# Performance work log

Measured on AMD Instinct MI355X. Metric: run time of the kernel, lower is better.

Reference implementation:

```python
import jax, jax.numpy as jnp
import numpy as np

N_NODES = 100000
N_EDGES = 400000
N_GRAPHS = 2048
F_IN = 78
HEADS1 = 10
OUT2 = 128


def _gat_conv(x, src, dst, W, a_src, a_dst, b, heads, out_dim):
    """PyG-style GATConv with self-loops already included in (src, dst)."""
    N = x.shape[0]
    h = (x @ W).reshape(N, heads, out_dim)                       # [N,H,D]
    alpha_src = jnp.einsum('nhd,hd->nh', h, a_src)               # [N,H]
    alpha_dst = jnp.einsum('nhd,hd->nh', h, a_dst)               # [N,H]
    e = jax.nn.leaky_relu(alpha_src[src] + alpha_dst[dst], 0.2)  # [E,H]
    # ragged softmax over incoming edges per destination node
    m = jax.ops.segment_max(e, dst, num_segments=N)
    m = jnp.where(jnp.isfinite(m), m, 0.0)
    ex = jnp.exp(e - jax.lax.stop_gradient(m)[dst])
    denom = jax.ops.segment_sum(ex, dst, num_segments=N)
    alpha = ex / (denom[dst] + 1e-16)                            # [E,H]
    msg = h[src] * alpha[:, :, None]                             # [E,H,D]
    out = jax.ops.segment_sum(msg, dst, num_segments=N)          # [N,H,D]
    return out.reshape(N, heads * out_dim) + b


def setup_inputs() -> dict:
    key = jax.random.key(0)
    ks = jax.random.split(key, 24)
    p = lambda k, shape: (jax.random.normal(k, shape, dtype=jnp.float32) * 0.05)
    x = jax.random.normal(ks[0], (N_NODES, F_IN), dtype=jnp.float32)
    edge_index = jax.random.randint(ks[1], (2, N_EDGES), 0, N_NODES, dtype=jnp.int32)
    # sorted batch assignment guaranteeing every graph is non-empty
    batch = ((jnp.arange(N_NODES, dtype=jnp.int32) * N_GRAPHS) // N_NODES).astype(jnp.int32)
    target = jax.random.normal(ks[2], (N_GRAPHS, 1280), dtype=jnp.float32)
    return {
        'x': x, 'edge_index': edge_index, 'batch': batch, 'target': target,
        'W1': p(ks[3], (F_IN, HEADS1 * F_IN)),
        'a_src1': p(ks[4], (HEADS1, F_IN)),
        'a_dst1': p(ks[5], (HEADS1, F_IN)),
        'b1': jnp.zeros((HEADS1 * F_IN,), jnp.float32),
        'W2': p(ks[6], (HEADS1 * F_IN, OUT2)),
        'a_src2': p(ks[7], (1, OUT2)),
        'a_dst2': p(ks[8], (1, OUT2)),
        'b2': jnp.zeros((OUT2,), jnp.float32),
        'w_gate': p(ks[9], (OUT2, 1)),
        'b_gate': jnp.zeros((1,), jnp.float32),
        'W_xt': p(ks[10], (1280, 256)),
        'b_xt': jnp.zeros((256,), jnp.float32),
        'W_fc1': p(ks[11], (512, 1024)),
        'b_fc1': jnp.zeros((1024,), jnp.float32),
        'W_fc2': p(ks[12], (1024, 256)),
        'b_fc2': jnp.zeros((256,), jnp.float32),
        'W_out': p(ks[13], (256, 1)),
        'b_out': jnp.zeros((1,), jnp.float32),
    }


def reference(x, edge_index, batch, target, W1, a_src1, a_dst1, b1,
              W2, a_src2, a_dst2, b2, w_gate, b_gate, W_xt, b_xt,
              W_fc1, b_fc1, W_fc2, b_fc2, W_out, b_out):
    N = x.shape[0]
    loop = jnp.arange(N, dtype=edge_index.dtype)
    src = jnp.concatenate([edge_index[0], loop])   # add self-loops (PyG default)
    dst = jnp.concatenate([edge_index[1], loop])

    h = jax.nn.elu(_gat_conv(x, src, dst, W1, a_src1, a_dst1, b1, HEADS1, F_IN))
    h = _gat_conv(h, src, dst, W2, a_src2, a_dst2, b2, 1, OUT2)
    h = jax.nn.relu(h)                              # [N,128]

    # WeightedSumAndMax readout
    w = jax.nn.sigmoid(h @ w_gate + b_gate)         # [N,1]
    h_sum = jax.ops.segment_sum(h * w, batch, num_segments=N_GRAPHS)  # [B,128]
    h_max = jax.ops.segment_max(h, batch, num_segments=N_GRAPHS)     # [B,128]
    hg = jnp.concatenate([h_sum, h_max], axis=1)    # [B,256]

    xt = target @ W_xt + b_xt                       # [B,256]
    xc = jnp.concatenate([hg, xt], axis=1)          # [B,512]
    xc = jax.nn.relu(xc @ W_fc1 + b_fc1)
    xc = jax.nn.relu(xc @ W_fc2 + b_fc2)
    return xc @ W_out + b_out                       # [B,1]
```

## Files before the change

kernel.cpp:

```cpp
#include <hip/hip_runtime.h>
#include <cstdint>
#include <cstddef>

#define N_NODESC 100000
#define N_EDGESC 400000
#define N_GRAPHSC 2048
#define F_INC 78
#define HEADS1C 10
#define D1C 78
#define F1C 780
#define OUT2C 128
#define E_TOTC (N_EDGESC + N_NODESC)

typedef unsigned short ushort_t;
typedef __attribute__((ext_vector_type(8))) short short8;
typedef __attribute__((ext_vector_type(4))) float f32x4;
typedef __attribute__((ext_vector_type(4))) unsigned int uint4v;
union U4S8 { uint4v u; short8 s; };

static __device__ __forceinline__ float lrelu(float x){ return x > 0.f ? x : 0.2f*x; }

static __device__ __forceinline__ float elu_fast(float v){
  return (v > 0.f) ? v : (__expf(v) - 1.0f);
}

static __device__ __forceinline__ void bar_lds(){
  asm volatile("s_waitcnt lgkmcnt(0)" ::: "memory");
  __builtin_amdgcn_s_barrier();
}

static __device__ __forceinline__ unsigned short f2bf(float f){
  unsigned int u = __float_as_uint(f);
  unsigned int r = (u + 0x7fffu + ((u >> 16) & 1u)) >> 16;
  return (unsigned short)r;
}
static __device__ __forceinline__ float bf2f(unsigned short h){
  return __uint_as_float(((unsigned int)h) << 16);
}

__global__ void k_deg(const int* __restrict__ ei, int* __restrict__ deg){
  int e = blockIdx.x*256 + threadIdx.x;
  if (e >= E_TOTC) return;
  int dst = (e < N_EDGESC) ? ei[N_EDGESC + e] : (e - N_EDGESC);
  atomicAdd(&deg[dst], 1);
}

__global__ __launch_bounds__(1024) void k_scan1(const int* __restrict__ deg,
                                                int* __restrict__ rowptr,
                                                int* __restrict__ bsum){
  __shared__ int s[1024];
  int t = threadIdx.x, i = blockIdx.x*1024 + t;
  int v = (i < N_NODESC) ? deg[i] : 0;
  s[t] = v; __syncthreads();
  for (int d = 1; d < 1024; d <<= 1){
    int xv = (t >= d) ? s[t-d] : 0;
    __syncthreads();
    s[t] += xv;
    __syncthreads();
  }
  if (i < N_NODESC) rowptr[i+1] = s[t];
  if (t == 1023) bsum[blockIdx.x] = s[t];
}

__global__ void k_scan2(int* __restrict__ bsum, int* __restrict__ rowptr, int nb){
  if (threadIdx.x == 0 && blockIdx.x == 0){
    int run = 0;
    for (int b = 0; b < nb; b++){ int v = bsum[b]; bsum[b] = run; run += v; }
    rowptr[0] = 0;
  }
}

__global__ __launch_bounds__(1024) void k_scan3(int* __restrict__ rowptr,
                                                const int* __restrict__ bsum){
  int i = blockIdx.x*1024 + threadIdx.x;
  if (i < N_NODESC) rowptr[i+1] += bsum[blockIdx.x];
}

__global__ void k_scatter(const int* __restrict__ ei, const int* __restrict__ rowptr,
                          int* __restrict__ cnt, int* __restrict__ esrc){
  int e = blockIdx.x*256 + threadIdx.x;
  if (e >= E_TOTC) return;
  int src, dst;
  if (e < N_EDGESC){ src = ei[e]; dst = ei[N_EDGESC + e]; }
  else { src = dst = e - N_EDGESC; }
  int pos = rowptr[dst] + atomicAdd(&cnt[dst], 1);
  esrc[pos] = src;
}

__global__ void k_wa1(const float* __restrict__ W1, const float* __restrict__ a_src1,
                      const float* __restrict__ a_dst1, float* __restrict__ Wa1){
  int i = blockIdx.x*256 + threadIdx.x;
  if (i >= F_INC*2*HEADS1C) return;
  int d = i / (2*HEADS1C), c = i % (2*HEADS1C);
  const float* a = (c < HEADS1C) ? a_src1 : a_dst1;
  int h = (c < HEADS1C) ? c : c - HEADS1C;
  float s = 0.f;
  for (int j = 0; j < D1C; j++) s += W1[d*F1C + h*D1C + j] * a[h*D1C + j];
  Wa1[d*(2*HEADS1C) + c] = s;
}

__global__ __launch_bounds__(256) void k_att1(const float* __restrict__ x,
                                              const float* __restrict__ Wa1,
                                              float* __restrict__ att1){
  int n = blockIdx.x*256 + threadIdx.x;
  if (n >= N_NODESC) return;
  const float* xr = x + (size_t)n*F_INC;
  float acc[20];
  #pragma unroll
  for (int c = 0; c < 20; c++) acc[c] = 0.f;
  for (int d0 = 0; d0 < F_INC; d0 += 2){
    float2 xv = *(const float2*)(xr + d0);
    const float* w0 = Wa1 + d0*20;
    #pragma unroll
    for (int c = 0; c < 20; c++)
      acc[c] += xv.x*w0[c] + xv.y*w0[20 + c];
  }
  float* o = att1 + (size_t)n*20;
  #pragma unroll
  for (int j = 0; j < 10; j++){
    float2 ov; ov.x = acc[2*j]; ov.y = acc[2*j+1];
    *(float2*)(o + 2*j) = ov;
  }
}

__global__ __launch_bounds__(256) void k_stats1(const float* __restrict__ att1,
                                                const int* __restrict__ rowptr,
                                                const int* __restrict__ esrc,
                                                float* __restrict__ stat1){
  int n = blockIdx.x*256 + threadIdx.x;
  if (n >= N_NODESC) return;
  float ad[10];
  {
    const float* a = att1 + (size_t)n*20 + 10;
    #pragma unroll
    for (int j = 0; j < 5; j++){
      float2 v = *(const float2*)(a + 2*j);
      ad[2*j] = v.x; ad[2*j+1] = v.y;
    }
  }
  int b = rowptr[n], e = rowptr[n+1];
  float m[10];
  #pragma unroll
  for (int h = 0; h < 10; h++) m[h] = -1e30f;
  for (int p = b; p < e; p += 2){
    int s0 = esrc[p];
    int s1 = esrc[(p+1 < e) ? p+1 : p];
    float2 v0[5], v1[5];
    #pragma unroll
    for (int j = 0; j < 5; j++) v0[j] = *(const float2*)(att1 + (size_t)s0*20 + 2*j);
    #pragma unroll
    for (int j = 0; j < 5; j++) v1[j] = *(const float2*)(att1 + (size_t)s1*20 + 2*j);
    #pragma unroll
    for (int h = 0; h < 10; h++){
      float a0 = (h & 1) ? v0[h>>1].y : v0[h>>1].x;
      m[h] = fmaxf(m[h], lrelu(a0 + ad[h]));
    }
    if (p+1 < e){
      #pragma unroll
      for (int h = 0; h < 10; h++){
        float a1 = (h & 1) ? v1[h>>1].y : v1[h>>1].x;
        m[h] = fmaxf(m[h], lrelu(a1 + ad[h]));
      }
    }
  }
  float den[10];
  #pragma unroll
  for (int h = 0; h < 10; h++) den[h] = 0.f;
  for (int p = b; p < e; p += 2){
    int s0 = esrc[p];
    int s1 = esrc[(p+1 < e) ? p+1 : p];
    float2 v0[5], v1[5];
    #pragma unroll
    for (int j = 0; j < 5; j++) v0[j] = *(const float2*)(att1 + (size_t)s0*20 + 2*j);
    #pragma unroll
    for (int j = 0; j < 5; j++) v1[j] = *(const float2*)(att1 + (size_t)s1*20 + 2*j);
    #pragma unroll
    for (int h = 0; h < 10; h++){
      float a0 = (h & 1) ? v0[h>>1].y : v0[h>>1].x;
      den[h] += expf(lrelu(a0 + ad[h]) - m[h]);
    }
    if (p+1 < e){
      #pragma unroll
      for (int h = 0; h < 10; h++){
        float a1 = (h & 1) ? v1[h>>1].y : v1[h>>1].x;
        den[h] += expf(lrelu(a1 + ad[h]) - m[h]);
      }
    }
  }
  float* o = stat1 + (size_t)n*20;
  #pragma unroll
  for (int h = 0; h < 10; h++){
    o[h] = m[h];
    o[10 + h] = 1.f/(den[h] + 1e-16f);
  }
}

__global__ __launch_bounds__(64) void k_agg1(
    const float* __restrict__ x, const float* __restrict__ att1,
    const float* __restrict__ stat1, const int* __restrict__ rowptr,
    const int* __restrict__ esrc, ushort_t* __restrict__ zc, int base){
  __shared__ float xs[4][F_INC];
  __shared__ float al[4][HEADS1C];
  int n = base + blockIdx.x;
  int l = threadIdx.x;
  int b = rowptr[n], e = rowptr[n+1];
  float acc[13];
  #pragma unroll
  for (int k = 0; k < 13; k++) acc[k] = 0.f;
  int hk[13], dk[13];
  #pragma unroll
  for (int k = 0; k < 13; k++){ int f = l + 64*k; hk[k] = f/78; dk[k] = f%78; }
  float ad = 0.f, mm = 0.f, rd = 0.f;
  if (l < HEADS1C){
    ad = att1[n*20 + 10 + l];
    mm = stat1[n*20 + l];
    rd = stat1[n*20 + 10 + l];
  }
  for (int p = b; p < e; p += 4){
    int c = e - p; if (c > 4) c = 4;
    int ss[4];
    #pragma unroll
    for (int j = 0; j < 4; j++) ss[j] = esrc[p + (j < c ? j : 0)];
    if (l < 39){
      #pragma unroll
      for (int j = 0; j < 4; j++){
        float2 v = *(const float2*)(x + (size_t)ss[j]*F_INC + 2*l);
        xs[j][2*l] = v.x; xs[j][2*l+1] = v.y;
      }
    }
    if (l < HEADS1C){
      #pragma unroll
      for (int j = 0; j < 4; j++){
        float ev = lrelu(att1[ss[j]*20 + l] + ad);
        al[j][l] = (j < c) ? expf(ev - mm) * rd : 0.f;
      }
    }
    __syncthreads();
    #pragma unroll
    for (int k = 0; k < 13; k++){
      int f = l + 64*k;
      if (f < F1C){
        float s = al[0][hk[k]]*xs[0][dk[k]] + al[1][hk[k]]*xs[1][dk[k]]
                + al[2][hk[k]]*xs[2][dk[k]] + al[3][hk[k]]*xs[3][dk[k]];
        acc[k] += s;
      }
    }
    __syncthreads();
  }
  #pragma unroll
  for (int k = 0; k < 13; k++){
    int f = l + 64*k;
    if (f < F1C) zc[(size_t)blockIdx.x*F1C + f] = f2bf(acc[k]);
  }
}

__global__ void k_prepW1(const float* __restrict__ W1, ushort_t* __restrict__ W1t){
  int i = blockIdx.x*256 + threadIdx.x;
  if (i >= HEADS1C*80*96) return;
  int h = i / (80*96), rem = i % (80*96), n = rem / 96, k = rem % 96;
  float v = (n < D1C && k < F_INC) ? W1[(size_t)k*F1C + h*D1C + n] : 0.f;
  W1t[i] = f2bf(v);
}

__global__ void k_prepW2f(const float* __restrict__ W2, ushort_t* __restrict__ W2f){
  int i = blockIdx.x*256 + threadIdx.x;
  if (i >= HEADS1C*128*96) return;
  int h = i / (128*96), rem = i % (128*96), n = rem / 96, k = rem % 96;
  float v = (k < D1C) ? W2[(size_t)(h*D1C + k)*OUT2C + n] : 0.f;
  W2f[i] = f2bf(v);
}

__global__ void k_prepWt(const float* __restrict__ W, ushort_t* __restrict__ Wt,
                         int Kdim, int Ndim, int KB){
  int i = blockIdx.x*256 + threadIdx.x;
  if (i >= Ndim*KB) return;
  int n = i / KB, k = i % KB;
  float v = (k < Kdim) ? W[(size_t)k*Ndim + n] : 0.f;
  Wt[i] = f2bf(v);
}

__global__ void k_cast_bf(const float* __restrict__ in, ushort_t* __restrict__ o, int n){
  int i = blockIdx.x*256 + threadIdx.x;
  if (i < n) o[i] = f2bf(in[i]);
}

template<int BN, int NT, int KB, int KVAL, int ACT, bool HASBIAS>
__global__ __launch_bounds__(256) void mfma_gemm(
    const ushort_t* __restrict__ A, const ushort_t* __restrict__ Bt,
    const float* __restrict__ bias, ushort_t* __restrict__ C,
    int M, int N, int lda, int ldc,
    int zsA, int zsBt, int zsC, int zsBias)
{
  __shared__ unsigned int As[64][20];
  __shared__ unsigned int Bs[BN][20];
  int z = blockIdx.z;
  A += (size_t)z*zsA; Bt += (size_t)z*zsBt; C += (size_t)z*zsC;
  const float* bz = HASBIAS ? (bias + (size_t)z*zsBias) : nullptr;
  int m0 = blockIdx.x*64;
  int n0 = blockIdx.y*BN;
  int t = threadIdx.x;
  int w = t >> 6, lane = t & 63;
  int q = lane >> 4, li = lane & 15;
  f32x4 acc[NT];
  #pragma unroll
  for (int i = 0; i < NT; i++) acc[i] = (f32x4){0.f,0.f,0.f,0.f};

  int am = t >> 2;
  int ak0 = (t & 3)*8;
  int gm = m0 + am;
  bool rv = (gm < M);

  #pragma unroll
  for (int ki = 0; ki < KB/32; ki++){
    const int kt = ki*32;
    int nv;
    if (ki == KB/32 - 1){
      int d = KVAL - ak0; nv = d < 0 ? 0 : (d > 8 ? 8 : d);
    } else nv = 8;
    {
      unsigned u0=0u, u1=0u, u2=0u, u3=0u;
      if (rv && nv > 0){
        const unsigned int* ap = (const unsigned int*)(A + (size_t)gm*lda + kt + ak0);
        u0 = ap[0]; u1 = ap[1]; u2 = ap[2]; u3 = ap[3];
        int ndw = nv >> 1;
        if (ndw < 4) u3 = 0u;
        if (ndw < 3) u2 = 0u;
        if (ndw < 2) u1 = 0u;
      }
      int c0 = (t & 3)*4;
      As[am][c0] = u0; As[am][c0+1] = u1; As[am][c0+2] = u2; As[am][c0+3] = u3;
    }
    for (int g = t; g < BN*4; g += 256){
      int n = g >> 2, c0 = (g & 3)*4;
      const unsigned int* bp = (const unsigned int*)(Bt + (size_t)(n0 + n)*KB + kt + c0*2);
      Bs[n][c0] = bp[0]; Bs[n][c0+1] = bp[1]; Bs[n][c0+2] = bp[2]; Bs[n][c0+3] = bp[3];
    }
    __syncthreads();
    U4S8 a; a.u = *(const uint4v*)&As[w*16 + li][q*4];
    #pragma unroll
    for (int nt = 0; nt < NT; nt++){
      U4S8 b; b.u = *(const uint4v*)&Bs[nt*16 + li][q*4];
      acc[nt] = __builtin_amdgcn_mfma_f32_16x16x32_bf16(a.s, b.s, acc[nt], 0, 0, 0);
    }
    __syncthreads();
  }
  #pragma unroll
  for (int nt = 0; nt < NT; nt++){
    int col = n0 + nt*16 + li;
    if (col >= N) continue;
    float bv = HASBIAS ? bz[col] : 0.f;
    #pragma unroll
    for (int r = 0; r < 4; r++){
      int gmr = m0 + w*16 + q*4 + r;
      if (gmr >= M) continue;
      float v = acc[nt][r] + bv;
      if (ACT == 1) v = fmaxf(v, 0.f);
      else if (ACT == 2) v = (v > 0.f) ? v : (__expf(v) - 1.0f);
      C[(size_t)gmr*ldc + col] = f2bf(v);
    }
  }
}

__global__ __launch_bounds__(256, 3) void mfma_fused12(
    const ushort_t* __restrict__ zc, const ushort_t* __restrict__ W1t,
    const float* __restrict__ b1, const ushort_t* __restrict__ W2f,
    ushort_t* __restrict__ h2pre, float* __restrict__ att2,
    const float* __restrict__ a_src2, const float* __restrict__ a_dst2,
    int M)
{
  __shared__ unsigned int Bs[128][52];
  __shared__ unsigned int Ts[64][52];
  int m0 = blockIdx.x*64;
  int t = threadIdx.x;
  int w = t >> 6, lane = t & 63;
  int q = lane >> 4, li = lane & 15;

  const uint4v* w1v = (const uint4v*)W1t;
  const uint4v* w2v = (const uint4v*)W2f;

  uint4v rw1[4], rw2[6];
  auto issueW1 = [&](int h){
    #pragma unroll
    for (int g0 = 0; g0 < 4; g0++){
      int g = t + g0*256;
      if (g < 960) rw1[g0] = w1v[(size_t)h*960 + g];
    }
  };
  auto writeW1 = [&](){
    #pragma unroll
    for (int g0 = 0; g0 < 4; g0++){
      int g = t + g0*256;
      if (g < 960){
        int n = g/12, c0 = (g%12)*4;
        *(uint4v*)&Bs[n][c0] = rw1[g0];
      }
    }
  };
  auto issueW2 = [&](int h){
    #pragma unroll
    for (int g0 = 0; g0 < 6; g0++)
      rw2[g0] = w2v[(size_t)h*1536 + t + g0*256];
  };
  auto writeW2 = [&](){
    #pragma unroll
    for (int g0 = 0; g0 < 6; g0++){
      int g = t + g0*256;
      int n = g/12, c0 = (g%12)*4;
      *(uint4v*)&Bs[n][c0] = rw2[g0];
    }
  };

  f32x4 acc2[8];
  #pragma unroll
  for (int i = 0; i < 8; i++) acc2[i] = (f32x4){0.f,0.f,0.f,0.f};

  issueW1(0);

  for (int i = t; i < 64*9; i += 256) Ts[i/9][39 + i%9] = 0u;

  int ar = m0 + w*16 + li;
  bool rv = (ar < M);
  const unsigned int* abase = (const unsigned int*)(zc + (size_t)ar*F1C);

  auto lda = [&](int h, uint4v* af){
    af[0] = (uint4v){0u,0u,0u,0u};
    af[1] = (uint4v){0u,0u,0u,0u};
    af[2] = (uint4v){0u,0u,0u,0u};
    if (rv){
      const unsigned int* p = abase + h*39 + q*4;
      af[0][0]=p[0];  af[0][1]=p[1];  af[0][2]=p[2];  af[0][3]=p[3];
      af[1][0]=p[16]; af[1][1]=p[17]; af[1][2]=p[18]; af[1][3]=p[19];
      if (q < 2){
        af[2][0]=p[32]; af[2][1]=p[33]; af[2][2]=p[34]; af[2][3]=p[35];
        if (q == 1) af[2][3] = 0u;
      }
    }
  };

  uint4v acur[3], anxt[3];
  lda(0, acur);

  #pragma unroll 1
  for (int h = 0; h < HEADS1C; h++){
    bar_lds();
    writeW1();
    issueW2(h);
    float bv[5];
    #pragma unroll
    for (int nt = 0; nt < 5; nt++){
      int col = nt*16 + li;
      bv[nt] = (col < D1C) ? b1[h*D1C + col] : 0.f;
    }
    bar_lds();

    f32x4 acc1[5];
    #pragma unroll
    for (int i = 0; i < 5; i++) acc1[i] = (f32x4){0.f,0.f,0.f,0.f};
    #pragma unroll
    for (int ki = 0; ki < 3; ki++){
      U4S8 a; a.u = acur[ki];
      #pragma unroll
      for (int nt = 0; nt < 5; nt++){
        U4S8 b; b.u = *(const uint4v*)&Bs[nt*16 + li][ki*16 + q*4];
        acc1[nt] = __builtin_amdgcn_mfma_f32_16x16x32_bf16(a.s, b.s, acc1[nt], 0, 0, 0);
      }
    }
    #pragma unroll
    for (int nt = 0; nt < 5; nt++){
      int col = nt*16 + li;
      #pragma unroll
      for (int r = 0; r < 4; r++){
        int row = w*16 + q*4 + r;
        float v = elu_fast(acc1[nt][r] + bv[nt]);
        ((ushort_t*)&Ts[row][0])[col] = f2bf(v);
      }
    }
    lda(h+1 < HEADS1C ? h+1 : 0, anxt);

    bar_lds();
    writeW2();
    issueW1(h+1 < HEADS1C ? h+1 : 0);
    bar_lds();

    #pragma unroll
    for (int ki = 0; ki < 3; ki++){
      U4S8 a; a.u = *(const uint4v*)&Ts[w*16 + li][ki*16 + q*4];
      #pragma unroll
      for (int nt = 0; nt < 8; nt++){
        U4S8 b; b.u = *(const uint4v*)&Bs[nt*16 + li][ki*16 + q*4];
        acc2[nt] = __builtin_amdgcn_mfma_f32_16x16x32_bf16(a.s, b.s, acc2[nt], 0, 0, 0);
      }
    }
    acur[0] = anxt[0]; acur[1] = anxt[1]; acur[2] = anxt[2];
  }

  float as2[8], ad2[8];
  #pragma unroll
  for (int nt = 0; nt < 8; nt++){
    int col = nt*16 + li;
    as2[nt] = a_src2[col];
    ad2[nt] = a_dst2[col];
  }
  #pragma unroll
  for (int r = 0; r < 4; r++){
    int gmr = m0 + w*16 + q*4 + r;
    float p0 = 0.f, p1 = 0.f;
    ushort_t hv[8];
    #pragma unroll
    for (int nt = 0; nt < 8; nt++){
      ushort_t hb = f2bf(acc2[nt][r]);
      float vb = bf2f(hb);
      p0 += vb*as2[nt]; p1 += vb*ad2[nt];
      hv[nt] = hb;
    }
    #pragma unroll
    for (int off = 1; off < 16; off <<= 1){
      p0 += __shfl_xor(p0, off);
      p1 += __shfl_xor(p1, off);
    }
    if (gmr < M){
      #pragma unroll
      for (int nt = 0; nt < 8; nt++)
        h2pre[(size_t)gmr*OUT2C + nt*16 + li] = hv[nt];
      if (li == 0){
        att2[(size_t)gmr*2]     = p0;
        att2[(size_t)gmr*2 + 1] = p1;
      }
    }
  }
}

__global__ void k_stats2(const float* __restrict__ att2, const int* __restrict__ rowptr,
                         const int* __restrict__ esrc, float* __restrict__ stat2){
  int n = blockIdx.x*256 + threadIdx.x;
  if (n >= N_NODESC) return;
  float ad = att2[n*2+1];
  int b = rowptr[n], e = rowptr[n+1];
  float m = -1e30f;
  for (int p = b; p < e; p += 4){
    int c = e - p; if (c > 4) c = 4;
    float v[4];
    #pragma unroll
    for (int j = 0; j < 4; j++){ int s = esrc[p + (j < c ? j : 0)]; v[j] = att2[s*2]; }
    #pragma unroll
    for (int j = 0; j < 4; j++) if (j < c) m = fmaxf(m, lrelu(v[j] + ad));
  }
  float den = 0.f;
  for (int p = b; p < e; p += 4){
    int c = e - p; if (c > 4) c = 4;
    float v[4];
    #pragma unroll
    for (int j = 0; j < 4; j++){ int s = esrc[p + (j < c ? j : 0)]; v[j] = att2[s*2]; }
    #pragma unroll
    for (int j = 0; j < 4; j++) if (j < c) den += expf(lrelu(v[j] + ad) - m);
  }
  stat2[n*2] = m;
  stat2[n*2+1] = 1.f/(den + 1e-16f);
}

__global__ void k_agg2(const ushort_t* __restrict__ h2pre,
                       const float* __restrict__ att2,
                       const float* __restrict__ stat2, const int* __restrict__ rowptr,
                       const int* __restrict__ esrc, const float* __restrict__ b2,
                       const float* __restrict__ w_gate, const float* __restrict__ b_gate,
                       float* __restrict__ h2, float* __restrict__ wnode){
  int n = blockIdx.x*4 + (threadIdx.x >> 6);
  int l = threadIdx.x & 63;
  if (n >= N_NODESC) return;
  float ad = att2[n*2+1], m = stat2[n*2], rd = stat2[n*2+1];
  int b = rowptr[n], e = rowptr[n+1];
  float a0 = 0.f, a1 = 0.f;
  for (int p = b; p < e; p += 4){
    int c = e - p; if (c > 4) c = 4;
    int ss[4];
    #pragma unroll
    for (int j = 0; j < 4; j++) ss[j] = esrc[p + (j < c ? j : 0)];
    unsigned u[4]; float at[4];
    #pragma unroll
    for (int j = 0; j < 4; j++) u[j] = *(const unsigned*)(h2pre + (size_t)ss[j]*OUT2C + 2*l);
    #pragma unroll
    for (int j = 0; j < 4; j++) at[j] = att2[ss[j]*2];
    #pragma unroll
    for (int j = 0; j < 4; j++){
      if (j < c){
        float alpha = expf(lrelu(at[j] + ad) - m) * rd;
        a0 += alpha * bf2f((ushort_t)(u[j] & 0xffffu));
        a1 += alpha * bf2f((ushort_t)(u[j] >> 16));
      }
    }
  }
  float v0 = fmaxf(a0 + b2[2*l],   0.f);
  float v1 = fmaxf(a1 + b2[2*l+1], 0.f);
  float2 hv; hv.x = v0; hv.y = v1;
  *(float2*)(h2 + (size_t)n*OUT2C + 2*l) = hv;
  float pp = v0*w_gate[2*l] + v1*w_gate[2*l+1];
  #pragma unroll
  for (int off = 32; off; off >>= 1) pp += __shfl_xor(pp, off);
  if (l == 0) wnode[n] = 1.f/(1.f + expf(-(pp + b_gate[0])));
}

__global__ __launch_bounds__(128) void k_readout(const float* __restrict__ h2,
                                                 const float* __restrict__ wnode,
                                                 const int* __restrict__ batch,
                                                 ushort_t* __restrict__ xcb){
  __shared__ int lohi[2];
  int g = blockIdx.x, t = threadIdx.x;
  if (t == 0){
    int lo = 0, hi = N_NODESC;
    while (lo < hi){ int mid = (lo+hi) >> 1; if (batch[mid] < g) lo = mid+1; else hi = mid; }
    lohi[0] = lo;
    int lo2 = lo; hi = N_NODESC;
    while (lo2 < hi){ int mid = (lo2+hi) >> 1; if (batch[mid] < g+1) lo2 = mid+1; else hi = mid; }
    lohi[1] = lo2;
  }
  __syncthreads();
  int lo = lohi[0], hi = lohi[1];
  float sum = 0.f, mx = 0.f;
  for (int n = lo; n < hi; n++){
    float v = h2[(size_t)n*OUT2C + t];
    sum += v * wnode[n];
    mx = fmaxf(mx, v);
  }
  xcb[(size_t)g*512 + t] = f2bf(sum);
  xcb[(size_t)g*512 + 128 + t] = f2bf(mx);
}

__global__ void k_final(const ushort_t* __restrict__ f2b, const float* __restrict__ W_out,
                        const float* __restrict__ b_out, float* __restrict__ out){
  int g = blockIdx.x*4 + (threadIdx.x >> 6);
  int l = threadIdx.x & 63;
  if (g >= N_GRAPHSC) return;
  float s = 0.f;
  #pragma unroll
  for (int k = 0; k < 4; k++) s += bf2f(f2b[(size_t)g*256 + l + 64*k]) * W_out[l + 64*k];
  #pragma unroll
  for (int off = 32; off; off >>= 1) s += __shfl_xor(s, off);
  if (l == 0) out[g] = s + b_out[0];
}

extern "C" void kernel_launch(void* const* d_in, const int* in_sizes, int n_in,
                              void* d_out, int out_size, void* d_ws, size_t ws_size,
                              hipStream_t stream) {
  const float* x      = (const float*)d_in[0];
  const int*   ei     = (const int*)d_in[1];
  const int*   batch  = (const int*)d_in[2];
  const float* target = (const float*)d_in[3];
  const float* W1     = (const float*)d_in[4];
  const float* a_src1 = (const float*)d_in[5];
  const float* a_dst1 = (const float*)d_in[6];
  const float* b1     = (const float*)d_in[7];
  const float* W2     = (const float*)d_in[8];
  const float* a_src2 = (const float*)d_in[9];
  const float* a_dst2 = (const float*)d_in[10];
  const float* b2     = (const float*)d_in[11];
  const float* w_gate = (const float*)d_in[12];
  const float* b_gate = (const float*)d_in[13];
  const float* W_xt   = (const float*)d_in[14];
  const float* b_xt   = (const float*)d_in[15];
  const float* W_fc1  = (const float*)d_in[16];
  const float* b_fc1  = (const float*)d_in[17];
  const float* W_fc2  = (const float*)d_in[18];
  const float* b_fc2  = (const float*)d_in[19];
  const float* W_out  = (const float*)d_in[20];
  const float* b_out  = (const float*)d_in[21];
  float* out = (float*)d_out;

  const size_t MB = (size_t)1 << 20;
  int C;
  if      (ws_size >= 245*MB) C = 1;
  else if (ws_size >= 150*MB) C = 2;
  else                        C = 4;
  const int R = N_NODESC / C;

  char* p = (char*)d_ws;
  auto carve = [&](size_t bytes) -> char* {
    char* r = p; p += (bytes + 255) & ~(size_t)255; return r;
  };
  int*   deg    = (int*)  carve((size_t)N_NODESC*4);
  int*   rowptr = (int*)  carve((size_t)(N_NODESC+1)*4);
  int*   cnt    = (int*)  carve((size_t)N_NODESC*4);
  int*   esrc   = (int*)  carve((size_t)E_TOTC*4);
  int*   bsum   = (int*)  carve(128*4);
  float* Wa1    = (float*)carve((size_t)F_INC*20*4);
  float* att1   = (float*)carve((size_t)N_NODESC*20*4);
  float* stat1  = (float*)carve((size_t)N_NODESC*20*4);
  float* att2   = (float*)carve((size_t)N_NODESC*2*4);
  float* stat2  = (float*)carve((size_t)N_NODESC*2*4);
  float* wnode  = (float*)carve((size_t)N_NODESC*4);
  ushort_t* W1t   = (ushort_t*)carve((size_t)HEADS1C*80*96*2);
  ushort_t* W2f   = (ushort_t*)carve((size_t)HEADS1C*128*96*2);
  ushort_t* Wxtt  = (ushort_t*)carve((size_t)256*1280*2);
  ushort_t* Wfc1t = (ushort_t*)carve((size_t)1024*512*2);
  ushort_t* Wfc2t = (ushort_t*)carve((size_t)256*1024*2);
  ushort_t* tb    = (ushort_t*)carve((size_t)N_GRAPHSC*1280*2);
  ushort_t* h2pre = (ushort_t*)carve((size_t)N_NODESC*OUT2C*2);
  ushort_t* xcb   = (ushort_t*)carve((size_t)N_GRAPHSC*512*2);
  ushort_t* f1b   = (ushort_t*)carve((size_t)N_GRAPHSC*1024*2);
  ushort_t* f2b   = (ushort_t*)carve((size_t)N_GRAPHSC*256*2);
  size_t big_bytes = (size_t)R*F1C*2 + 4096;
  size_t h2_bytes  = (size_t)N_NODESC*OUT2C*4;
  char*  BIG = carve(big_bytes > h2_bytes ? big_bytes : h2_bytes);
  ushort_t* zc  = (ushort_t*)BIG;
  float* h2 = (float*)BIG;

  hipMemsetAsync(deg, 0, (size_t)N_NODESC*4, stream);
  hipMemsetAsync(cnt, 0, (size_t)N_NODESC*4, stream);

  k_deg<<<(E_TOTC+255)/256, 256, 0, stream>>>(ei, deg);
  int nb = (N_NODESC + 1023)/1024;
  k_scan1<<<nb, 1024, 0, stream>>>(deg, rowptr, bsum);
  k_scan2<<<1, 64, 0, stream>>>(bsum, rowptr, nb);
  k_scan3<<<nb, 1024, 0, stream>>>(rowptr, bsum);
  k_scatter<<<(E_TOTC+255)/256, 256, 0, stream>>>(ei, rowptr, cnt, esrc);

  k_prepW1<<<(HEADS1C*80*96+255)/256, 256, 0, stream>>>(W1, W1t);
  k_prepW2f<<<(HEADS1C*128*96+255)/256, 256, 0, stream>>>(W2, W2f);
  k_prepWt<<<(256*1280+255)/256, 256, 0, stream>>>(W_xt, Wxtt, 1280, 256, 1280);
  k_prepWt<<<(1024*512+255)/256, 256, 0, stream>>>(W_fc1, Wfc1t, 512, 1024, 512);
  k_prepWt<<<(256*1024+255)/256, 256, 0, stream>>>(W_fc2, Wfc2t, 1024, 256, 1024);
  k_cast_bf<<<((N_GRAPHSC*1280)+255)/256, 256, 0, stream>>>(target, tb, N_GRAPHSC*1280);

  k_wa1<<<(F_INC*20+255)/256, 256, 0, stream>>>(W1, a_src1, a_dst1, Wa1);
  k_att1<<<(N_NODESC+255)/256, 256, 0, stream>>>(x, Wa1, att1);
  k_stats1<<<(N_NODESC+255)/256, 256, 0, stream>>>(att1, rowptr, esrc, stat1);

  for (int c = 0; c < C; c++){
    int base = c*R;
    k_agg1<<<R, 64, 0, stream>>>(x, att1, stat1, rowptr, esrc, zc, base);
    mfma_fused12<<<(R+63)/64, 256, 0, stream>>>(
        zc, W1t, b1, W2f, h2pre + (size_t)base*OUT2C, att2 + (size_t)base*2,
        a_src2, a_dst2, R);
  }

  k_stats2<<<(N_NODESC+255)/256, 256, 0, stream>>>(att2, rowptr, esrc, stat2);
  k_agg2<<<(N_NODESC+3)/4, 256, 0, stream>>>(h2pre, att2, stat2, rowptr, esrc,
                                             b2, w_gate, b_gate, h2, wnode);

  k_readout<<<N_GRAPHSC, 128, 0, stream>>>(h2, wnode, batch, xcb);
  mfma_gemm<128,8,1280,32,0,true><<<dim3(N_GRAPHSC/64, 256/128, 1), 256, 0, stream>>>(
      tb, Wxtt, b_xt, xcb + 256, N_GRAPHSC, 256, 1280, 512, 0,0,0,0);
  mfma_gemm<128,8,512,32,1,true><<<dim3(N_GRAPHSC/64, 1024/128, 1), 256, 0, stream>>>(
      xcb, Wfc1t, b_fc1, f1b, N_GRAPHSC, 1024, 512, 1024, 0,0,0,0);
  mfma_gemm<128,8,1024,32,1,true><<<dim3(N_GRAPHSC/64, 256/128, 1), 256, 0, stream>>>(
      f1b, Wfc2t, b_fc2, f2b, N_GRAPHSC, 256, 1024, 256, 0,0,0,0);
  k_final<<<(N_GRAPHSC+3)/4, 256, 0, stream>>>(f2b, W_out, b_out, out);
}
```

Measured before the change: 629.3 us.

## Pack four nodes per k_agg1 block and double-buffer W1/W2 LDS in fused GEMM

k_agg1 now runs four destination nodes per 256-thread block, one per wave. Each wave keeps its own LDS slices, so the block-wide __syncthreads become a wave-local lgkmcnt wait, which cuts launch count and raises occupancy. mfma_fused12 gives W1 and W2 separate LDS buffers, so each weight load overlaps the other GEMM phase and each head needs two barriers instead of four. This costs more LDS per block, and the new k_agg1 grid assumes R is divisible by four.

```diff
diff --git a/kernel.cpp b/kernel.cpp
--- a/kernel.cpp
+++ b/kernel.cpp
@@ -27,6 +27,10 @@
 static __device__ __forceinline__ void bar_lds(){
   asm volatile("s_waitcnt lgkmcnt(0)" ::: "memory");
   __builtin_amdgcn_s_barrier();
+}
+
+static __device__ __forceinline__ void wave_lds_fence(){
+  asm volatile("s_waitcnt lgkmcnt(0)" ::: "memory");
 }
 
 static __device__ __forceinline__ unsigned short f2bf(float f){
@@ -195,14 +199,16 @@
   }
 }
 
-__global__ __launch_bounds__(64) void k_agg1(
+__global__ __launch_bounds__(256) void k_agg1(
     const float* __restrict__ x, const float* __restrict__ att1,
     const float* __restrict__ stat1, const int* __restrict__ rowptr,
     const int* __restrict__ esrc, ushort_t* __restrict__ zc, int base){
-  __shared__ float xs[4][F_INC];
-  __shared__ float al[4][HEADS1C];
-  int n = base + blockIdx.x;
-  int l = threadIdx.x;
+  __shared__ float xs[4][4][F_INC];
+  __shared__ float al[4][4][HEADS1C];
+  int wv = threadIdx.x >> 6;
+  int l  = threadIdx.x & 63;
+  int nl = blockIdx.x*4 + wv;
+  int n  = base + nl;
   int b = rowptr[n], e = rowptr[n+1];
   float acc[13];
   #pragma unroll
@@ -225,32 +231,32 @@
       #pragma unroll
       for (int j = 0; j < 4; j++){
         float2 v = *(const float2*)(x + (size_t)ss[j]*F_INC + 2*l);
-        xs[j][2*l] = v.x; xs[j][2*l+1] = v.y;
+        xs[wv][j][2*l] = v.x; xs[wv][j][2*l+1] = v.y;
       }
     }
     if (l < HEADS1C){
       #pragma unroll
       for (int j = 0; j < 4; j++){
         float ev = lrelu(att1[ss[j]*20 + l] + ad);
-        al[j][l] = (j < c) ? expf(ev - mm) * rd : 0.f;
-      }
-    }
-    __syncthreads();
+        al[wv][j][l] = (j < c) ? expf(ev - mm) * rd : 0.f;
+      }
+    }
+    wave_lds_fence();
     #pragma unroll
     for (int k = 0; k < 13; k++){
       int f = l + 64*k;
       if (f < F1C){
-        float s = al[0][hk[k]]*xs[0][dk[k]] + al[1][hk[k]]*xs[1][dk[k]]
-                + al[2][hk[k]]*xs[2][dk[k]] + al[3][hk[k]]*xs[3][dk[k]];
+        float s = al[wv][0][hk[k]]*xs[wv][0][dk[k]] + al[wv][1][hk[k]]*xs[wv][1][dk[k]]
+                + al[wv][2][hk[k]]*xs[wv][2][dk[k]] + al[wv][3][hk[k]]*xs[wv][3][dk[k]];
         acc[k] += s;
       }
     }
-    __syncthreads();
+    asm volatile("" ::: "memory");
   }
   #pragma unroll
   for (int k = 0; k < 13; k++){
     int f = l + 64*k;
-    if (f < F1C) zc[(size_t)blockIdx.x*F1C + f] = f2bf(acc[k]);
+    if (f < F1C) zc[(size_t)nl*F1C + f] = f2bf(acc[k]);
   }
 }
 
@@ -368,7 +374,8 @@
     const float* __restrict__ a_src2, const float* __restrict__ a_dst2,
     int M)
 {
-  __shared__ unsigned int Bs[128][52];
+  __shared__ unsigned int Bs1[80*48];
+  __shared__ unsigned int Bs2[128*48];
   __shared__ unsigned int Ts[64][52];
   int m0 = blockIdx.x*64;
   int t = threadIdx.x;
@@ -390,10 +397,7 @@
     #pragma unroll
     for (int g0 = 0; g0 < 4; g0++){
       int g = t + g0*256;
-      if (g < 960){
-        int n = g/12, c0 = (g%12)*4;
-        *(uint4v*)&Bs[n][c0] = rw1[g0];
-      }
+      if (g < 960) *(uint4v*)&Bs1[g*4] = rw1[g0];
     }
   };
   auto issueW2 = [&](int h){
@@ -405,8 +409,7 @@
     #pragma unroll
     for (int g0 = 0; g0 < 6; g0++){
       int g = t + g0*256;
-      int n = g/12, c0 = (g%12)*4;
-      *(uint4v*)&Bs[n][c0] = rw2[g0];
+      *(uint4v*)&Bs2[g*4] = rw2[g0];
     }
   };
 
@@ -415,6 +418,7 @@
   for (int i = 0; i < 8; i++) acc2[i] = (f32x4){0.f,0.f,0.f,0.f};
 
   issueW1(0);
+  issueW2(0);
 
   for (int i = t; i < 64*9; i += 256) Ts[i/9][39 + i%9] = 0u;
 
@@ -440,18 +444,20 @@
   uint4v acur[3], anxt[3];
   lda(0, acur);
 
+  writeW1();
+  bar_lds();
+
   #pragma unroll 1
   for (int h = 0; h < HEADS1C; h++){
-    bar_lds();
-    writeW1();
-    issueW2(h);
+    int hn = (h+1 < HEADS1C) ? h+1 : 0;
+    writeW2();
+    issueW1(hn);
     float bv[5];
     #pragma unroll
     for (int nt = 0; nt < 5; nt++){
       int col = nt*16 + li;
       bv[nt] = (col < D1C) ? b1[h*D1C + col] : 0.f;
     }
-    bar_lds();
 
     f32x4 acc1[5];
     #pragma unroll
@@ -461,7 +467,7 @@
       U4S8 a; a.u = acur[ki];
       #pragma unroll
       for (int nt = 0; nt < 5; nt++){
-        U4S8 b; b.u = *(const uint4v*)&Bs[nt*16 + li][ki*16 + q*4];
+        U4S8 b; b.u = *(const uint4v*)&Bs1[(nt*16 + li)*48 + ki*16 + q*4];
         acc1[nt] = __builtin_amdgcn_mfma_f32_16x16x32_bf16(a.s, b.s, acc1[nt], 0, 0, 0);
       }
     }
@@ -475,22 +481,22 @@
         ((ushort_t*)&Ts[row][0])[col] = f2bf(v);
       }
     }
-    lda(h+1 < HEADS1C ? h+1 : 0, anxt);
+    lda(hn, anxt);
 
     bar_lds();
-    writeW2();
-    issueW1(h+1 < HEADS1C ? h+1 : 0);
-    bar_lds();
+    writeW1();
+    issueW2(hn);
 
     #pragma unroll
     for (int ki = 0; ki < 3; ki++){
       U4S8 a; a.u = *(const uint4v*)&Ts[w*16 + li][ki*16 + q*4];
       #pragma unroll
       for (int nt = 0; nt < 8; nt++){
-        U4S8 b; b.u = *(const uint4v*)&Bs[nt*16 + li][ki*16 + q*4];
+        U4S8 b; b.u = *(const uint4v*)&Bs2[(nt*16 + li)*48 + ki*16 + q*4];
         acc2[nt] = __builtin_amdgcn_mfma_f32_16x16x32_bf16(a.s, b.s, acc2[nt], 0, 0, 0);
       }
     }
+    bar_lds();
     acur[0] = anxt[0]; acur[1] = anxt[1]; acur[2] = anxt[2];
   }
 
@@ -726,7 +732,7 @@
 
   for (int c = 0; c < C; c++){
     int base = c*R;
-    k_agg1<<<R, 64, 0, stream>>>(x, att1, stat1, rowptr, esrc, zc, base);
+    k_agg1<<<R/4, 256, 0, stream>>>(x, att1, stat1, rowptr, esrc, zc, base);
     mfma_fused12<<<(R+63)/64, 256, 0, stream>>>(
         zc, W1t, b1, W2f, h2pre + (size_t)base*OUT2C, att2 + (size_t)base*2,
         a_src2, a_dst2, R);
```

New measurement: 653.4 us. +3.8%, slower.
